# Performance work log

Measured on AMD Instinct MI355X. Metric: run time of the kernel, lower is better.

Reference implementation:

```python
import jax, jax.numpy as jnp
import numpy as np

MARGIN = 1.0


def setup_inputs() -> dict:
    key = jax.random.key(0)
    k1, k2 = jax.random.split(key)
    B, D, K = 2048, 256, 8
    scores = jax.random.normal(k1, (B, D), dtype=jnp.float32)
    pos_indices = jax.random.randint(k2, (B, K), 0, D, dtype=jnp.int64)
    return {"scores": scores, "pos_indices": pos_indices, "num_developers": D}


def reference(scores, pos_indices, num_developers):
    B, D = scores.shape
    # boolean positive mask per sample (duplicate indices collapse like a set)
    pos_mask = jnp.zeros((B, D), dtype=scores.dtype)
    pos_mask = pos_mask.at[jnp.arange(B)[:, None], pos_indices].set(1.0)
    neg_mask = 1.0 - pos_mask
    # all-pairs hinge: relu(s_neg - s_pos + margin), masked to (neg, pos) pairs
    # diff[b, n, p] = scores[b, n] - scores[b, p] + margin
    diff = scores[:, :, None] - scores[:, None, :] + MARGIN
    pair_mask = neg_mask[:, :, None] * pos_mask[:, None, :]
    loss_sum = jnp.sum(jax.nn.relu(diff) * pair_mask)
    num_pairs = jnp.sum(pair_mask)
    # original returns 0.0 when there are no (pos, neg) pairs
    return jnp.where(num_pairs > 0, loss_sum / jnp.maximum(num_pairs, 1.0), 0.0)
```

## Files before the change

kernel.cpp:

```cpp
#include <hip/hip_runtime.h>

#define TPB 256

template <int KC>
__device__ inline void accum_samples(const float* __restrict__ scores,
                                     const int* __restrict__ idx,
                                     int D, int B, int K,
                                     float& loss, float& pairs) {
    for (int b = blockIdx.x; b < B; b += gridDim.x) {
        const int rbase = b * D;
        const int ibase = b * K;

        if (KC > 0) {
            int   ik[KC > 0 ? KC : 1];
            float ps[KC > 0 ? KC : 1];
            int   validmask = 0, P = 0;
#pragma unroll
            for (int k = 0; k < KC; ++k) ik[k] = idx[ibase + k];
#pragma unroll
            for (int k = 0; k < KC; ++k) {
                bool dup = false;
#pragma unroll
                for (int j = 0; j < KC; ++j)
                    if (j < k) dup |= (ik[j] == ik[k]);
                if (!dup) { validmask |= (1 << k); ++P; }
                ps[k] = scores[rbase + ik[k]];
            }
            for (int d = threadIdx.x; d < D; d += TPB) {
                const float s = scores[rbase + d] + 1.0f;
                bool is_pos = false;
#pragma unroll
                for (int k = 0; k < KC; ++k) is_pos |= (ik[k] == d);
                if (!is_pos) {
#pragma unroll
                    for (int k = 0; k < KC; ++k) {
                        if (validmask & (1 << k)) {
                            float v = s - ps[k];
                            loss += (v > 0.0f) ? v : 0.0f;
                        }
                    }
                }
            }
            if (threadIdx.x == 0) pairs += (float)((D - P) * P);
        } else {
            int P = 0;
            for (int k = 0; k < K; ++k) {
                bool dup = false;
                for (int j = 0; j < k; ++j) dup |= (idx[ibase + j] == idx[ibase + k]);
                if (!dup) ++P;
            }
            for (int d = threadIdx.x; d < D; d += TPB) {
                const float s = scores[rbase + d] + 1.0f;
                bool is_pos = false;
                for (int k = 0; k < K; ++k) is_pos |= (idx[ibase + k] == d);
                if (!is_pos) {
                    for (int k = 0; k < K; ++k) {
                        bool dup = false;
                        for (int j = 0; j < k; ++j) dup |= (idx[ibase + j] == idx[ibase + k]);
                        if (!dup) {
                            float v = s - scores[rbase + idx[ibase + k]];
                            loss += (v > 0.0f) ? v : 0.0f;
                        }
                    }
                }
            }
            if (threadIdx.x == 0) pairs += (float)((D - P) * P);
        }
    }
}

__global__ __launch_bounds__(TPB) void mlrl_main(
        const float* __restrict__ scores,
        const int* __restrict__ idx,
        const int* __restrict__ ndev,
        int total_scores, int total_idx,
        float2* __restrict__ partials) {
    const int D = *ndev;
    const int B = total_scores / D;
    const int K = total_idx / B;

    float loss = 0.0f, pairs = 0.0f;
    if (K == 8) accum_samples<8>(scores, idx, D, B, K, loss, pairs);
    else        accum_samples<0>(scores, idx, D, B, K, loss, pairs);

    for (int off = 32; off > 0; off >>= 1) {
        loss  += __shfl_down(loss,  off);
        pairs += __shfl_down(pairs, off);
    }
    __shared__ float2 red[TPB / 64];
    const int wave = threadIdx.x >> 6;
    const int lane = threadIdx.x & 63;
    if (lane == 0) red[wave] = make_float2(loss, pairs);
    __syncthreads();
    if (threadIdx.x == 0) {
        float2 acc = red[0];
        for (int w = 1; w < TPB / 64; ++w) { acc.x += red[w].x; acc.y += red[w].y; }
        partials[blockIdx.x] = acc;
    }
}

__global__ __launch_bounds__(TPB) void mlrl_finalize(
        const float2* __restrict__ partials, int n, float* __restrict__ out) {
    double l = 0.0, p = 0.0;
    for (int i = threadIdx.x; i < n; i += blockDim.x) {
        float2 v = partials[i];
        l += (double)v.x;
        p += (double)v.y;
    }
    for (int off = 32; off > 0; off >>= 1) {
        l += __shfl_down(l, off);
        p += __shfl_down(p, off);
    }
    __shared__ double sl[TPB / 64], sp[TPB / 64];
    const int wave = threadIdx.x >> 6;
    const int lane = threadIdx.x & 63;
    if (lane == 0) { sl[wave] = l; sp[wave] = p; }
    __syncthreads();
    if (threadIdx.x == 0) {
        double L = 0.0, P = 0.0;
        for (int w = 0; w < TPB / 64; ++w) { L += sl[w]; P += sp[w]; }
        out[0] = (P > 0.0) ? (float)(L / (P < 1.0 ? 1.0 : P)) : 0.0f;
    }
}

extern "C" void kernel_launch(void* const* d_in, const int* in_sizes, int n_in,
                              void* d_out, int out_size, void* d_ws, size_t ws_size,
                              hipStream_t stream) {
    const float* scores = (const float*)d_in[0];
    const int*   idx    = (const int*)d_in[1];
    const int*   ndev   = (const int*)d_in[2];
    float* out = (float*)d_out;

    const int total_scores = in_sizes[0];
    const int total_idx    = in_sizes[1];

    int nblocks = total_scores / 256;
    if (nblocks < 1) nblocks = 1;
    if ((size_t)nblocks * sizeof(float2) > ws_size)
        nblocks = (int)(ws_size / sizeof(float2));

    float2* partials = (float2*)d_ws;

    mlrl_main<<<nblocks, TPB, 0, stream>>>(scores, idx, ndev,
                                           total_scores, total_idx, partials);
    mlrl_finalize<<<1, TPB, 0, stream>>>(partials, nblocks, out);
}
```

Measured before the change: 65.03 us.

## Fuse reduction into one kernel with wave-per-sample and atomic last-block finalize

Replaces the two-kernel main+finalize scheme with a single kernel in which each wavefront handles one sample using float4 loads and precomputed (1 - pos score) constants, branch-free via -inf masking. The final reduction uses double atomics plus a block counter, so the last block writes the result. This removes one kernel launch and the partials pass, and cuts per-sample block overhead, but adds a memset before the launch and atomic contention on the accumulators.

```diff
diff --git a/kernel.cpp b/kernel.cpp
--- a/kernel.cpp
+++ b/kernel.cpp
@@ -1,125 +1,124 @@
 #include <hip/hip_runtime.h>
+#include <math.h>
 
 #define TPB 256
+#define WPB (TPB / 64)
 
-template <int KC>
-__device__ inline void accum_samples(const float* __restrict__ scores,
-                                     const int* __restrict__ idx,
-                                     int D, int B, int K,
-                                     float& loss, float& pairs) {
-    for (int b = blockIdx.x; b < B; b += gridDim.x) {
-        const int rbase = b * D;
-        const int ibase = b * K;
+__global__ __launch_bounds__(TPB) void mlrl_fused(
+        const float* __restrict__ scores,
+        const int*   __restrict__ idx,
+        const int*   __restrict__ ndev,
+        int total_scores, int total_idx,
+        double* __restrict__ accs,
+        unsigned int* __restrict__ counter,
+        int nblk,
+        float* __restrict__ out) {
 
-        if (KC > 0) {
-            int   ik[KC > 0 ? KC : 1];
-            float ps[KC > 0 ? KC : 1];
-            int   validmask = 0, P = 0;
-#pragma unroll
-            for (int k = 0; k < KC; ++k) ik[k] = idx[ibase + k];
-#pragma unroll
-            for (int k = 0; k < KC; ++k) {
+    const int D    = *ndev;
+    const int lane = threadIdx.x & 63;
+    const int wv = __builtin_amdgcn_readfirstlane((int)threadIdx.x) >> 6;
+    const int gw      = blockIdx.x * WPB + wv;
+    const int gstride = gridDim.x * WPB;
+
+    float loss = 0.0f, pairs = 0.0f;
+
+    const bool fast = (D == 256) &&
+                      ((long long)total_idx * 32LL == (long long)total_scores) &&
+                      ((total_scores & 255) == 0);
+
+    if (fast) {
+        const int B = total_scores >> 8;
+        for (int b = gw; b < B; b += gstride) {
+            const int rb = b << 8;
+            const int ib = b << 3;
+
+            const int4 i0 = *reinterpret_cast<const int4*>(idx + ib);
+            const int4 i1 = *reinterpret_cast<const int4*>(idx + ib + 4);
+            int ik[8] = { i0.x, i0.y, i0.z, i0.w, i1.x, i1.y, i1.z, i1.w };
+
+            const float4 v = *reinterpret_cast<const float4*>(scores + rb + (lane << 2));
+
+            float c[8];
+            int P = 0;
+            #pragma unroll
+            for (int k = 0; k < 8; ++k) {
                 bool dup = false;
-#pragma unroll
-                for (int j = 0; j < KC; ++j)
+                #pragma unroll
+                for (int j = 0; j < 8; ++j)
                     if (j < k) dup |= (ik[j] == ik[k]);
-                if (!dup) { validmask |= (1 << k); ++P; }
-                ps[k] = scores[rbase + ik[k]];
+                const float pscore = scores[rb + ik[k]];
+                if (!dup) { ++P; c[k] = 1.0f - pscore; }
+                else      { c[k] = -INFINITY; }
             }
-            for (int d = threadIdx.x; d < D; d += TPB) {
-                const float s = scores[rbase + d] + 1.0f;
-                bool is_pos = false;
-#pragma unroll
-                for (int k = 0; k < KC; ++k) is_pos |= (ik[k] == d);
-                if (!is_pos) {
-#pragma unroll
-                    for (int k = 0; k < KC; ++k) {
-                        if (validmask & (1 << k)) {
-                            float v = s - ps[k];
-                            loss += (v > 0.0f) ? v : 0.0f;
+
+            const int e0 = lane << 2;
+            const float se[4] = { v.x, v.y, v.z, v.w };
+            #pragma unroll
+            for (int j = 0; j < 4; ++j) {
+                const int e = e0 + j;
+                bool pos = false;
+                #pragma unroll
+                for (int k = 0; k < 8; ++k) pos |= (ik[k] == e);
+                const float s = pos ? -INFINITY : se[j];
+                #pragma unroll
+                for (int k = 0; k < 8; ++k)
+                    loss += fmaxf(0.0f, s + c[k]);
+            }
+            if (lane == 0) pairs += (float)((256 - P) * P);
+        }
+    } else if (D > 0) {
+        const int B = total_scores / D;
+        const int K = (B > 0) ? (total_idx / B) : 0;
+        for (int b = gw; b < B; b += gstride) {
+            const int rb = b * D, ib = b * K;
+            int P = 0;
+            for (int k = 0; k < K; ++k) {
+                bool dup = false;
+                for (int j = 0; j < k; ++j) dup |= (idx[ib + j] == idx[ib + k]);
+                if (!dup) ++P;
+            }
+            for (int d = lane; d < D; d += 64) {
+                const float s = scores[rb + d] + 1.0f;
+                bool pos = false;
+                for (int k = 0; k < K; ++k) pos |= (idx[ib + k] == d);
+                if (!pos) {
+                    for (int k = 0; k < K; ++k) {
+                        bool dup = false;
+                        for (int j = 0; j < k; ++j) dup |= (idx[ib + j] == idx[ib + k]);
+                        if (!dup) {
+                            const float t = s - scores[rb + idx[ib + k]];
+                            loss += (t > 0.0f) ? t : 0.0f;
                         }
                     }
                 }
             }
-            if (threadIdx.x == 0) pairs += (float)((D - P) * P);
-        } else {
-            int P = 0;
-            for (int k = 0; k < K; ++k) {
-                bool dup = false;
-                for (int j = 0; j < k; ++j) dup |= (idx[ibase + j] == idx[ibase + k]);
-                if (!dup) ++P;
-            }
-            for (int d = threadIdx.x; d < D; d += TPB) {
-                const float s = scores[rbase + d] + 1.0f;
-                bool is_pos = false;
-                for (int k = 0; k < K; ++k) is_pos |= (idx[ibase + k] == d);
-                if (!is_pos) {
-                    for (int k = 0; k < K; ++k) {
-                        bool dup = false;
-                        for (int j = 0; j < k; ++j) dup |= (idx[ibase + j] == idx[ibase + k]);
-                        if (!dup) {
-                            float v = s - scores[rbase + idx[ibase + k]];
-                            loss += (v > 0.0f) ? v : 0.0f;
-                        }
-                    }
-                }
-            }
-            if (threadIdx.x == 0) pairs += (float)((D - P) * P);
+            if (lane == 0) pairs += (float)((D - P) * P);
         }
     }
-}
 
-__global__ __launch_bounds__(TPB) void mlrl_main(
-        const float* __restrict__ scores,
-        const int* __restrict__ idx,
-        const int* __restrict__ ndev,
-        int total_scores, int total_idx,
-        float2* __restrict__ partials) {
-    const int D = *ndev;
-    const int B = total_scores / D;
-    const int K = total_idx / B;
+    #pragma unroll
+    for (int off = 32; off > 0; off >>= 1)
+        loss += __shfl_down(loss, off, 64);
 
-    float loss = 0.0f, pairs = 0.0f;
-    if (K == 8) accum_samples<8>(scores, idx, D, B, K, loss, pairs);
-    else        accum_samples<0>(scores, idx, D, B, K, loss, pairs);
+    __shared__ float2 red[WPB];
+    if (lane == 0) red[wv] = make_float2(loss, pairs);
+    __syncthreads();
 
-    for (int off = 32; off > 0; off >>= 1) {
-        loss  += __shfl_down(loss,  off);
-        pairs += __shfl_down(pairs, off);
-    }
-    __shared__ float2 red[TPB / 64];
-    const int wave = threadIdx.x >> 6;
-    const int lane = threadIdx.x & 63;
-    if (lane == 0) red[wave] = make_float2(loss, pairs);
-    __syncthreads();
     if (threadIdx.x == 0) {
-        float2 acc = red[0];
-        for (int w = 1; w < TPB / 64; ++w) { acc.x += red[w].x; acc.y += red[w].y; }
-        partials[blockIdx.x] = acc;
-    }
-}
+        float L = red[0].x, Pp = red[0].y;
+        #pragma unroll
+        for (int w = 1; w < WPB; ++w) { L += red[w].x; Pp += red[w].y; }
 
-__global__ __launch_bounds__(TPB) void mlrl_finalize(
-        const float2* __restrict__ partials, int n, float* __restrict__ out) {
-    double l = 0.0, p = 0.0;
-    for (int i = threadIdx.x; i < n; i += blockDim.x) {
-        float2 v = partials[i];
-        l += (double)v.x;
-        p += (double)v.y;
-    }
-    for (int off = 32; off > 0; off >>= 1) {
-        l += __shfl_down(l, off);
-        p += __shfl_down(p, off);
-    }
-    __shared__ double sl[TPB / 64], sp[TPB / 64];
-    const int wave = threadIdx.x >> 6;
-    const int lane = threadIdx.x & 63;
-    if (lane == 0) { sl[wave] = l; sp[wave] = p; }
-    __syncthreads();
-    if (threadIdx.x == 0) {
-        double L = 0.0, P = 0.0;
-        for (int w = 0; w < TPB / 64; ++w) { L += sl[w]; P += sp[w]; }
-        out[0] = (P > 0.0) ? (float)(L / (P < 1.0 ? 1.0 : P)) : 0.0f;
+        atomicAdd(&accs[0], (double)L);
+        atomicAdd(&accs[1], (double)Pp);
+        __threadfence();
+        const unsigned prev = atomicAdd(counter, 1u);
+        if (prev == (unsigned)nblk - 1u) {
+            __threadfence();
+            const double l = atomicAdd(&accs[0], 0.0);
+            const double p = atomicAdd(&accs[1], 0.0);
+            out[0] = (p > 0.0) ? (float)(l / (p < 1.0 ? 1.0 : p)) : 0.0f;
+        }
     }
 }
 
@@ -129,19 +128,20 @@
     const float* scores = (const float*)d_in[0];
     const int*   idx    = (const int*)d_in[1];
     const int*   ndev   = (const int*)d_in[2];
-    float* out = (float*)d_out;
 
     const int total_scores = in_sizes[0];
     const int total_idx    = in_sizes[1];
 
-    int nblocks = total_scores / 256;
-    if (nblocks < 1) nblocks = 1;
-    if ((size_t)nblocks * sizeof(float2) > ws_size)
-        nblocks = (int)(ws_size / sizeof(float2));
+    double*       accs    = (double*)d_ws;
+    unsigned int* counter = (unsigned int*)((char*)d_ws + 16);
 
-    float2* partials = (float2*)d_ws;
+    hipMemsetAsync(d_ws, 0, 32, stream);
 
-    mlrl_main<<<nblocks, TPB, 0, stream>>>(scores, idx, ndev,
-                                           total_scores, total_idx, partials);
-    mlrl_finalize<<<1, TPB, 0, stream>>>(partials, nblocks, out);
+    int nblk = total_scores >> 10;
+    if (nblk < 1)    nblk = 1;
+    if (nblk > 2048) nblk = 2048;
+
+    mlrl_fused<<<nblk, TPB, 0, stream>>>(scores, idx, ndev,
+                                         total_scores, total_idx,
+                                         accs, counter, nblk, (float*)d_out);
 }
```

Measured after the change: 79.84 us. 1.23x slower.
